# Kernel tuning notes

Measured on AMD Instinct MI355X. Metric: run time of the kernel, lower is better.

## Reference

```python
import jax, jax.numpy as jnp
import numpy as np
from jax import lax

B, PR, PC, IN, E, H = 32, 32, 32, 256, 256, 512  # H2 = 2*H = GRU hidden
H2 = 2 * H
EPS = 1e-5


def setup_inputs() -> dict:
    key = jax.random.key(0)
    ks = jax.random.split(key, 8)
    s = 0.02
    return {
        "x": jax.random.normal(ks[0], (B, PR, PC, IN), jnp.float32),
        "emb_W": jax.random.normal(ks[1], (E, IN), jnp.float32) * s,
        "emb_b": jnp.zeros((E,), jnp.float32),
        "W_ih": jax.random.normal(ks[2], (3 * H2, E), jnp.float32) * s,
        "b_ih": jnp.zeros((3 * H2,), jnp.float32),
        "W_hh": jax.random.normal(ks[3], (3 * H2, H2), jnp.float32) * s,
        "b_hh": jnp.zeros((3 * H2,), jnp.float32),
        "comp_W": jax.random.normal(ks[4], (H, H2), jnp.float32) * s,
        "comp_b": jnp.zeros((H,), jnp.float32),
        "res_W": jax.random.normal(ks[5], (H, E), jnp.float32) * s,
        "res_b": jnp.zeros((H,), jnp.float32),
        "ln_g": jnp.ones((H,), jnp.float32),
        "ln_b": jnp.zeros((H,), jnp.float32),
    }


def reference(x, emb_W, emb_b, W_ih, b_ih, W_hh, b_hh, comp_W, comp_b,
              res_W, res_b, ln_g, ln_b):
    # Embed all cells at once, then precompute input-side GRU gates and residual proj.
    e = jnp.einsum('bijd,ed->bije', x, emb_W) + emb_b          # (B,PR,PC,E)
    gi = jnp.einsum('bije,ge->bijg', e, W_ih) + b_ih            # (B,PR,PC,3*H2)
    res = jnp.einsum('bije,he->bije'.replace('e->','h->')[:0] or 'bije,he->bijh', e, res_W) + res_b  # (B,PR,PC,H)

    def cell(last_col, inputs):
        gi_c, res_c, last_row_c = inputs        # (B,3H2), (B,H), (B,H)
        h_prev = jnp.concatenate([last_row_c, last_col], axis=-1)  # (B,H2)
        gh = h_prev @ W_hh.T + b_hh                                 # (B,3H2)
        ir, iz, inn = jnp.split(gi_c, 3, axis=-1)
        hr, hz, hn = jnp.split(gh, 3, axis=-1)
        r = jax.nn.sigmoid(ir + hr)
        z = jax.nn.sigmoid(iz + hz)
        n = jnp.tanh(inn + r * hn)
        h = (1.0 - z) * n + z * h_prev                              # (B,H2) GRU cell out
        hc = h @ comp_W.T + comp_b + res_c                          # compress + residual
        mu = jnp.mean(hc, axis=-1, keepdims=True)
        var = jnp.var(hc, axis=-1, keepdims=True)
        hn_out = (hc - mu) / jnp.sqrt(var + EPS) * ln_g + ln_b      # LayerNorm
        return hn_out, hn_out

    def row_step(prev_row, row_inputs):
        gi_r, res_r = row_inputs                 # (PC,B,3H2), (PC,B,H)
        last_rows = jnp.swapaxes(prev_row, 0, 1)  # (PC,B,H)
        init_col = jnp.zeros((x.shape[0], H), x.dtype)
        _, row_out = lax.scan(cell, init_col, (gi_r, res_r, last_rows))  # (PC,B,H)
        new_row = jnp.swapaxes(row_out, 0, 1)     # (B,PC,H)
        return new_row, new_row

    gi_s = jnp.transpose(gi, (1, 2, 0, 3))    # (PR,PC,B,3H2)
    res_s = jnp.transpose(res, (1, 2, 0, 3))  # (PR,PC,B,H)
    init_row = jnp.zeros((x.shape[0], x.shape[2], H), x.dtype)
    _, rows = lax.scan(row_step, init_row, (gi_s, res_s))  # (PR,B,PC,H)

    output = jnp.transpose(rows, (1, 0, 2, 3))[None]  # (1,B,PR,PC,H)
    h_final = output[0, :, -1, -1, :]                 # (B,H)
    return output, h_final
```

## Files before the change

kernel.cpp:

```cpp
#include <hip/hip_runtime.h>
#include <hip/hip_fp16.h>

typedef _Float16 h8 __attribute__((ext_vector_type(8)));
typedef _Float16 h4 __attribute__((ext_vector_type(4)));
typedef float f4 __attribute__((ext_vector_type(4)));

#define DEV __device__ __forceinline__

constexpr unsigned kNumBlk = 256u;

DEV float sigm(float x) { return 1.f / (1.f + __expf(-x)); }
DEV float tanhfast(float x) {
    x = fminf(fmaxf(x, -15.f), 15.f);
    float e = __expf(2.f * x);
    return (e - 1.f) / (e + 1.f);
}
DEV h8 h8zero() {
    h8 v;
#pragma unroll
    for (int e = 0; e < 8; ++e) v[e] = (_Float16)0.f;
    return v;
}

DEV void gbar(unsigned* bar, unsigned nblocks) {
    __syncthreads();
    if (threadIdx.x == 0) {
        __threadfence();
        unsigned g = __hip_atomic_load(&bar[1], __ATOMIC_RELAXED, __HIP_MEMORY_SCOPE_AGENT);
        unsigned prev = __hip_atomic_fetch_add(&bar[0], 1u, __ATOMIC_RELAXED, __HIP_MEMORY_SCOPE_AGENT);
        if (prev + 1u == nblocks) {
            __hip_atomic_store(&bar[0], 0u, __ATOMIC_RELAXED, __HIP_MEMORY_SCOPE_AGENT);
            __hip_atomic_store(&bar[1], g + 1u, __ATOMIC_RELEASE, __HIP_MEMORY_SCOPE_AGENT);
        } else {
            unsigned cur;
            do {
                __builtin_amdgcn_s_sleep(2);
                cur = __hip_atomic_load(&bar[1], __ATOMIC_RELAXED, __HIP_MEMORY_SCOPE_AGENT);
            } while (cur == g);
        }
        (void)__hip_atomic_load(&bar[1], __ATOMIC_ACQUIRE, __HIP_MEMORY_SCOPE_AGENT);
    }
    __syncthreads();
}

__global__ void k_zero(unsigned* ptr, int n) {
    int i = blockIdx.x * 256 + threadIdx.x;
    if (i < n) ptr[i] = 0u;
}

__global__ void k_cast_f2h(const float* __restrict__ in, _Float16* __restrict__ out, int n4) {
    int i = blockIdx.x * blockDim.x + threadIdx.x;
    if (i < n4) {
        float4 v = reinterpret_cast<const float4*>(in)[i];
        h4 o;
        o[0] = (_Float16)v.x; o[1] = (_Float16)v.y; o[2] = (_Float16)v.z; o[3] = (_Float16)v.w;
        reinterpret_cast<h4*>(out)[i] = o;
    }
}

__global__ void k_pack_wext(const float* __restrict__ Wih, const float* __restrict__ Whh,
                            _Float16* __restrict__ Wext) {
    int n = blockIdx.x, g = n >> 10, kk = n & 1023;
#pragma unroll
    for (int it = 0; it < 5; ++it) {
        int k = it * 256 + threadIdx.x;
        float v;
        if (k < 1024) v = (g == 3) ? 0.f : Whh[(size_t)(g * 1024 + kk) * 1024 + k];
        else          v = (g == 2) ? 0.f : Wih[(size_t)((g == 3 ? 2048 + kk : g * 1024 + kk)) * 256 + (k - 1024)];
        Wext[(size_t)n * 1280 + k] = (_Float16)v;
    }
}

__global__ void k_pack_cwext(const float* __restrict__ compW, const float* __restrict__ resW,
                             _Float16* __restrict__ cWext) {
    int n = blockIdx.x;
#pragma unroll
    for (int it = 0; it < 5; ++it) {
        int k = it * 256 + threadIdx.x;
        float v = (k < 1024) ? compW[(size_t)n * 1024 + k] : resW[(size_t)n * 256 + (k - 1024)];
        cWext[(size_t)n * 1280 + k] = (_Float16)v;
    }
}

__global__ __launch_bounds__(256, 1) void k_gemm_a32(
    const float* __restrict__ A, const _Float16* __restrict__ W,
    const float* __restrict__ bias, _Float16* __restrict__ C,
    int M, int N, int K, int Ntiles) {
    __shared__ __align__(16) _Float16 sA[128 * 72];
    __shared__ __align__(16) _Float16 sB[128 * 72];
    int tm = blockIdx.x / Ntiles, tn = blockIdx.x % Ntiles;
    int tid = threadIdx.x, lane = tid & 63, w = tid >> 6;
    int wr = w >> 1, wc = w & 1;
    f4 acc[4][4] = {};
    for (int k0 = 0; k0 < K; k0 += 64) {
#pragma unroll
        for (int p = 0; p < 4; ++p) {
            int ch = tid + p * 256;
            int r = ch >> 3, cc = ch & 7;
            const float* ap = A + (size_t)(tm * 128 + r) * K + k0 + cc * 8;
            float4 v0 = *reinterpret_cast<const float4*>(ap);
            float4 v1 = *reinterpret_cast<const float4*>(ap + 4);
            h8 va;
            va[0] = (_Float16)v0.x; va[1] = (_Float16)v0.y; va[2] = (_Float16)v0.z; va[3] = (_Float16)v0.w;
            va[4] = (_Float16)v1.x; va[5] = (_Float16)v1.y; va[6] = (_Float16)v1.z; va[7] = (_Float16)v1.w;
            *reinterpret_cast<h8*>(sA + r * 72 + cc * 8) = va;
            h8 vb = *reinterpret_cast<const h8*>(W + (size_t)(tn * 128 + r) * K + k0 + cc * 8);
            *reinterpret_cast<h8*>(sB + r * 72 + cc * 8) = vb;
        }
        __syncthreads();
#pragma unroll
        for (int kc = 0; kc < 2; ++kc) {
            int ro = lane & 15;
            int ko = kc * 32 + (lane >> 4) * 8;
            h8 af[4], bf[4];
#pragma unroll
            for (int mf = 0; mf < 4; ++mf)
                af[mf] = *reinterpret_cast<const h8*>(sA + (wr * 64 + mf * 16 + ro) * 72 + ko);
#pragma unroll
            for (int nf = 0; nf < 4; ++nf)
                bf[nf] = *reinterpret_cast<const h8*>(sB + (wc * 64 + nf * 16 + ro) * 72 + ko);
#pragma unroll
            for (int mf = 0; mf < 4; ++mf)
#pragma unroll
                for (int nf = 0; nf < 4; ++nf)
                    acc[mf][nf] = __builtin_amdgcn_mfma_f32_16x16x32_f16(af[mf], bf[nf], acc[mf][nf], 0, 0, 0);
        }
        __syncthreads();
    }
#pragma unroll
    for (int nf = 0; nf < 4; ++nf) {
        int col = tn * 128 + wc * 64 + nf * 16 + (lane & 15);
        float bs = bias[col];
#pragma unroll
        for (int mf = 0; mf < 4; ++mf) {
#pragma unroll
            for (int q = 0; q < 4; ++q) {
                int row = tm * 128 + wr * 64 + mf * 16 + (lane >> 4) * 4 + q;
                C[(size_t)row * N + col] = (_Float16)(acc[mf][nf][q] + bs);
            }
        }
    }
}

struct SA { _Float16 A[128 * 72]; _Float16 B[128 * 72]; };
struct SB { _Float16 A[32 * 72]; _Float16 B[64 * 72]; float red[4][32][2]; };
union __align__(16) SM { SA a; SB b; };

__global__ __launch_bounds__(256, 1) void k_recur(
    const _Float16* __restrict__ e_h,
    const _Float16* __restrict__ Wext,
    const _Float16* __restrict__ cWext,
    const float* __restrict__ bih, const float* __restrict__ bhh,
    const float* __restrict__ compb, const float* __restrict__ resb,
    const float* __restrict__ lng, const float* __restrict__ lnb,
    _Float16* __restrict__ hbuf,
    float* __restrict__ out,
    float* __restrict__ hfinal,
    unsigned* bar,
    unsigned* ctr,
    float* gred) {
    __shared__ SM sm;
    const int tid = threadIdx.x, lane = tid & 63, w = tid >> 6;
    const int lane15 = lane & 15, hi = lane >> 4;

    for (int d = 0; d < 63; ++d) {
        int i0 = d > 31 ? d - 31 : 0;
        int i1 = d < 31 ? d : 31;
        int ncells = i1 - i0 + 1;
        int Mt = (ncells + 3) >> 2;

        if ((int)blockIdx.x < Mt * 32) {
            int s = blockIdx.x & 31;
            int mt = blockIdx.x >> 5;
            f4 acc[2][8] = {};
            for (int kt = 0; kt < 20; ++kt) {
                int k0 = kt * 64;
#pragma unroll
                for (int p = 0; p < 4; ++p) {
                    int ch = tid + p * 256;
                    int r = ch >> 3, cc = ch & 7;
                    int m = mt * 128 + r;
                    int c = m >> 5; if (c >= ncells) c = ncells - 1;
                    int b = m & 31;
                    int i = i0 + c, j = d - i;
                    int k = k0 + cc * 8;
                    h8 v;
                    if (k < 1024) {
                        const float* src = nullptr;
                        if (k < 512) {
                            if (i > 0) src = out + (((size_t)(((b * 32 + (i - 1)) * 32) + j)) << 9) + k;
                        } else {
                            if (j > 0) src = out + (((size_t)(((b * 32 + i) * 32) + (j - 1))) << 9) + (k - 512);
                        }
                        if (src) {
                            float4 f0 = *reinterpret_cast<const float4*>(src);
                            float4 f1 = *reinterpret_cast<const float4*>(src + 4);
                            v[0] = (_Float16)f0.x; v[1] = (_Float16)f0.y;
                            v[2] = (_Float16)f0.z; v[3] = (_Float16)f0.w;
                            v[4] = (_Float16)f1.x; v[5] = (_Float16)f1.y;
                            v[6] = (_Float16)f1.z; v[7] = (_Float16)f1.w;
                        } else v = h8zero();
                    } else {
                        v = *reinterpret_cast<const h8*>(e_h + ((size_t)((b * 32 + i) * 32 + j) << 8) + (k - 1024));
                    }
                    *reinterpret_cast<h8*>(sm.a.A + r * 72 + cc * 8) = v;
                }
#pragma unroll
                for (int p = 0; p < 4; ++p) {
                    int ch = tid + p * 256;
                    int rr = ch >> 3, cc = ch & 7;
                    int g = rr >> 5, t = rr & 31;
                    int n = g * 1024 + s * 32 + t;
                    h8 v = *reinterpret_cast<const h8*>(Wext + (size_t)n * 1280 + k0 + cc * 8);
                    *reinterpret_cast<h8*>(sm.a.B + rr * 72 + cc * 8) = v;
                }
                __syncthreads();
#pragma unroll
                for (int kc = 0; kc < 2; ++kc) {
                    int ko = kc * 32 + hi * 8;
                    h8 af[2], bf[8];
#pragma unroll
                    for (int mf = 0; mf < 2; ++mf)
                        af[mf] = *reinterpret_cast<const h8*>(sm.a.A + (w * 32 + mf * 16 + lane15) * 72 + ko);
#pragma unroll
                    for (int nf = 0; nf < 8; ++nf)
                        bf[nf] = *reinterpret_cast<const h8*>(sm.a.B + ((nf >> 1) * 32 + (nf & 1) * 16 + lane15) * 72 + ko);
#pragma unroll
                    for (int mf = 0; mf < 2; ++mf)
#pragma unroll
                        for (int nf = 0; nf < 8; ++nf)
                            acc[mf][nf] = __builtin_amdgcn_mfma_f32_16x16x32_f16(af[mf], bf[nf], acc[mf][nf], 0, 0, 0);
                }
                __syncthreads();
            }
#pragma unroll
            for (int mf = 0; mf < 2; ++mf) {
                int rbase = mt * 128 + w * 32 + mf * 16 + hi * 4;
#pragma unroll
                for (int q = 0; q < 4; ++q) {
                    int m = rbase + q;
                    int c = m >> 5;
                    if (c >= ncells) continue;
                    int b = m & 31;
                    int i = i0 + c, j = d - i;
#pragma unroll
                    for (int u = 0; u < 2; ++u) {
                        int kk = s * 32 + u * 16 + lane15;
                        float r_ = sigm(acc[mf][u][q] + bih[kk] + bhh[kk]);
                        float z_ = sigm(acc[mf][2 + u][q] + bih[1024 + kk] + bhh[1024 + kk]);
                        float hn_ = acc[mf][4 + u][q] + bhh[2048 + kk];
                        float in_ = acc[mf][6 + u][q] + bih[2048 + kk];
                        float hp;
                        if (kk < 512)
                            hp = (i == 0) ? 0.f
                                 : out[(((size_t)(((b * 32 + (i - 1)) * 32) + j)) << 9) + kk];
                        else
                            hp = (j == 0) ? 0.f
                                 : out[(((size_t)(((b * 32 + i) * 32) + (j - 1))) << 9) + kk - 512];
                        float n_ = tanhfast(in_ + r_ * hn_);
                        float h_ = (1.f - z_) * n_ + z_ * hp;
                        hbuf[((size_t)(c * 32 + b) << 10) + kk] = (_Float16)h_;
                    }
                }
            }
        }
        gbar(bar, kNumBlk);

        if ((int)blockIdx.x < ncells * 8) {
            int c = blockIdx.x >> 3, sl = blockIdx.x & 7;
            int i = i0 + c, j = d - i;
            f4 acc[2] = {};
            const _Float16* Ab = hbuf + ((size_t)c << 15);
            for (int kt = 0; kt < 20; ++kt) {
                int k0 = kt * 64;
                {
                    int r = tid >> 3, cc = tid & 7;
                    int k = k0 + cc * 8;
                    h8 v;
                    if (k < 1024) v = *reinterpret_cast<const h8*>(Ab + ((size_t)r << 10) + k);
                    else v = *reinterpret_cast<const h8*>(e_h + ((size_t)((r * 32 + i) * 32 + j) << 8) + (k - 1024));
                    *reinterpret_cast<h8*>(sm.b.A + r * 72 + cc * 8) = v;
                }
#pragma unroll
                for (int p = 0; p < 2; ++p) {
                    int ch = tid + p * 256;
                    int rr = ch >> 3, cc = ch & 7;
                    h8 v = *reinterpret_cast<const h8*>(cWext + (size_t)(sl * 64 + rr) * 1280 + k0 + cc * 8);
                    *reinterpret_cast<h8*>(sm.b.B + rr * 72 + cc * 8) = v;
                }
                __syncthreads();
#pragma unroll
                for (int kc = 0; kc < 2; ++kc) {
                    int ko = kc * 32 + hi * 8;
                    h8 bf = *reinterpret_cast<const h8*>(sm.b.B + (w * 16 + lane15) * 72 + ko);
#pragma unroll
                    for (int mf = 0; mf < 2; ++mf) {
                        h8 af = *reinterpret_cast<const h8*>(sm.b.A + (mf * 16 + lane15) * 72 + ko);
                        acc[mf] = __builtin_amdgcn_mfma_f32_16x16x32_f16(af, bf, acc[mf], 0, 0, 0);
                    }
                }
                __syncthreads();
            }
            int col = sl * 64 + w * 16 + lane15;
            float cb = compb[col] + resb[col];
            float s1[2][4], s2[2][4];
#pragma unroll
            for (int mf = 0; mf < 2; ++mf)
#pragma unroll
                for (int q = 0; q < 4; ++q) {
                    float v = acc[mf][q] + cb;
                    acc[mf][q] = v;
                    s1[mf][q] = v; s2[mf][q] = v * v;
                }
#pragma unroll
            for (int off = 1; off < 16; off <<= 1)
#pragma unroll
                for (int mf = 0; mf < 2; ++mf)
#pragma unroll
                    for (int q = 0; q < 4; ++q) {
                        s1[mf][q] += __shfl_xor(s1[mf][q], off, 64);
                        s2[mf][q] += __shfl_xor(s2[mf][q], off, 64);
                    }
            if (lane15 == 0)
#pragma unroll
                for (int mf = 0; mf < 2; ++mf)
#pragma unroll
                    for (int q = 0; q < 4; ++q) {
                        int b = mf * 16 + hi * 4 + q;
                        sm.b.red[w][b][0] = s1[mf][q];
                        sm.b.red[w][b][1] = s2[mf][q];
                    }
            __syncthreads();
            size_t gbase = (((size_t)d * 32 + c) << 6);
            if (tid < 32) {
                int b = tid;
                float t1 = sm.b.red[0][b][0] + sm.b.red[1][b][0] + sm.b.red[2][b][0] + sm.b.red[3][b][0];
                float t2 = sm.b.red[0][b][1] + sm.b.red[1][b][1] + sm.b.red[2][b][1] + sm.b.red[3][b][1];
                atomicAdd(&gred[gbase + b * 2 + 0], t1);
                atomicAdd(&gred[gbase + b * 2 + 1], t2);
            }
            if (tid == 0) {
                __hip_atomic_fetch_add(&ctr[d * 32 + c], 1u, __ATOMIC_RELEASE, __HIP_MEMORY_SCOPE_AGENT);
                unsigned cur;
                do {
                    __builtin_amdgcn_s_sleep(2);
                    cur = __hip_atomic_load(&ctr[d * 32 + c], __ATOMIC_RELAXED, __HIP_MEMORY_SCOPE_AGENT);
                } while (cur < 8u);
                (void)__hip_atomic_load(&ctr[d * 32 + c], __ATOMIC_ACQUIRE, __HIP_MEMORY_SCOPE_AGENT);
            }
            __syncthreads();
            float lg = lng[col], lb = lnb[col];
#pragma unroll
            for (int mf = 0; mf < 2; ++mf)
#pragma unroll
                for (int q = 0; q < 4; ++q) {
                    int b = mf * 16 + hi * 4 + q;
                    float t1 = gred[gbase + b * 2 + 0];
                    float t2 = gred[gbase + b * 2 + 1];
                    float mu = t1 * (1.f / 512.f);
                    float var = t2 * (1.f / 512.f) - mu * mu;
                    float rstd = rsqrtf(var + 1e-5f);
                    float y = (acc[mf][q] - mu) * rstd * lg + lb;
                    size_t ob = ((size_t)((b * 32 + i) * 32 + j)) << 9;
                    out[ob + col] = y;
                    if (i == 31 && j == 31) hfinal[((size_t)b << 9) + col] = y;
                }
            __syncthreads();
        }
        gbar(bar, kNumBlk);
    }
}

extern "C" void kernel_launch(void* const* d_in, const int* in_sizes, int n_in,
                              void* d_out, int out_size, void* d_ws, size_t ws_size,
                              hipStream_t stream) {
    const float* x = (const float*)d_in[0];
    const float* embW = (const float*)d_in[1];
    const float* embb = (const float*)d_in[2];
    const float* Wih = (const float*)d_in[3];
    const float* bih = (const float*)d_in[4];
    const float* Whh = (const float*)d_in[5];
    const float* bhh = (const float*)d_in[6];
    const float* compW = (const float*)d_in[7];
    const float* compb = (const float*)d_in[8];
    const float* resW = (const float*)d_in[9];
    const float* resb = (const float*)d_in[10];
    const float* lng = (const float*)d_in[11];
    const float* lnb = (const float*)d_in[12];
    float* out = (float*)d_out;
    float* hfinal = out + (size_t)32768 * 512;
    (void)in_sizes; (void)n_in; (void)out_size; (void)ws_size;

    _Float16* p = (_Float16*)d_ws;
    _Float16* e_h = p;    p += 8388608;
    _Float16* embW_h = p; p += 65536;
    _Float16* Wext = p;   p += 5242880;
    _Float16* cWext = p;  p += 655360;
    _Float16* hbuf = p;   p += 1048576;
    unsigned* bar = (unsigned*)p;
    unsigned* ctr = bar + 2;
    float* gred = (float*)(ctr + 63 * 32);
    const int kZeroWords = 2 + 63 * 32 + 63 * 32 * 32 * 2;

    k_zero<<<(kZeroWords + 255) / 256, 256, 0, stream>>>(bar, kZeroWords);
    k_cast_f2h<<<64, 256, 0, stream>>>(embW, embW_h, 16384);
    k_pack_wext<<<4096, 256, 0, stream>>>(Wih, Whh, Wext);
    k_pack_cwext<<<512, 256, 0, stream>>>(compW, resW, cWext);
    k_gemm_a32<<<512, 256, 0, stream>>>(x, embW_h, embb, e_h, 32768, 256, 256, 2);

    k_recur<<<dim3(kNumBlk), dim3(256), 0, stream>>>(
        e_h, Wext, cWext, bih, bhh, compb, resb, lng, lnb,
        hbuf, out, hfinal, bar, ctr, gred);
}
```

Baseline: 6.907 ms.

## Double grid to 512 blocks, add fp16 wavefront buffers, double-buffer tiles, hierarchical barrier

Doubles the persistent grid to 512 blocks with two blocks per CU and halves each block's GEMM tile, so a diagonal's work is spread over more blocks. The previous anti-diagonal's hidden states are stored in a compact fp16 ping-pong buffer, so they no longer have to be re-read from the fp32 output and converted. Both GEMM phases get register-staged double-buffered LDS loads to overlap global loads with MFMA. The grid barrier becomes two-level: eight groups of 64 blocks, then a final count, to reduce atomic contention. The cost is more barrier participants, a smaller tile per block, and the need for two blocks to fit in LDS and registers on each CU.

```diff
diff --git a/kernel.cpp b/kernel.cpp
--- a/kernel.cpp
+++ b/kernel.cpp
@@ -7,7 +7,8 @@
 
 #define DEV __device__ __forceinline__
 
-constexpr unsigned kNumBlk = 256u;
+constexpr unsigned kNumBlk = 512u;
+constexpr int kFrontSz = 32 * 32 * 512;
 
 DEV float sigm(float x) { return 1.f / (1.f + __expf(-x)); }
 DEV float tanhfast(float x) {
@@ -22,23 +23,26 @@
     return v;
 }
 
-DEV void gbar(unsigned* bar, unsigned nblocks) {
+DEV void gbar(unsigned* bar, int grp) {
     __syncthreads();
     if (threadIdx.x == 0) {
         __threadfence();
-        unsigned g = __hip_atomic_load(&bar[1], __ATOMIC_RELAXED, __HIP_MEMORY_SCOPE_AGENT);
-        unsigned prev = __hip_atomic_fetch_add(&bar[0], 1u, __ATOMIC_RELAXED, __HIP_MEMORY_SCOPE_AGENT);
-        if (prev + 1u == nblocks) {
-            __hip_atomic_store(&bar[0], 0u, __ATOMIC_RELAXED, __HIP_MEMORY_SCOPE_AGENT);
-            __hip_atomic_store(&bar[1], g + 1u, __ATOMIC_RELEASE, __HIP_MEMORY_SCOPE_AGENT);
-        } else {
-            unsigned cur;
-            do {
-                __builtin_amdgcn_s_sleep(2);
-                cur = __hip_atomic_load(&bar[1], __ATOMIC_RELAXED, __HIP_MEMORY_SCOPE_AGENT);
-            } while (cur == g);
-        }
-        (void)__hip_atomic_load(&bar[1], __ATOMIC_ACQUIRE, __HIP_MEMORY_SCOPE_AGENT);
+        unsigned g = __hip_atomic_load(&bar[9], __ATOMIC_RELAXED, __HIP_MEMORY_SCOPE_AGENT);
+        unsigned p = __hip_atomic_fetch_add(&bar[grp], 1u, __ATOMIC_ACQ_REL, __HIP_MEMORY_SCOPE_AGENT);
+        if (p == 63u) {
+            __hip_atomic_store(&bar[grp], 0u, __ATOMIC_RELAXED, __HIP_MEMORY_SCOPE_AGENT);
+            unsigned r = __hip_atomic_fetch_add(&bar[8], 1u, __ATOMIC_ACQ_REL, __HIP_MEMORY_SCOPE_AGENT);
+            if (r == 7u) {
+                __hip_atomic_store(&bar[8], 0u, __ATOMIC_RELAXED, __HIP_MEMORY_SCOPE_AGENT);
+                __hip_atomic_store(&bar[9], g + 1u, __ATOMIC_RELEASE, __HIP_MEMORY_SCOPE_AGENT);
+            }
+        }
+        unsigned cur;
+        do {
+            __builtin_amdgcn_s_sleep(2);
+            cur = __hip_atomic_load(&bar[9], __ATOMIC_RELAXED, __HIP_MEMORY_SCOPE_AGENT);
+        } while (cur == g);
+        (void)__hip_atomic_load(&bar[9], __ATOMIC_ACQUIRE, __HIP_MEMORY_SCOPE_AGENT);
     }
     __syncthreads();
 }
@@ -142,11 +146,11 @@
     }
 }
 
-struct SA { _Float16 A[128 * 72]; _Float16 B[128 * 72]; };
-struct SB { _Float16 A[32 * 72]; _Float16 B[64 * 72]; float red[4][32][2]; };
+struct SA { _Float16 A[2][64 * 72]; _Float16 B[2][128 * 72]; };
+struct SB { _Float16 A[2][32 * 72]; _Float16 B[2][32 * 72]; float red[4][32][2]; };
 union __align__(16) SM { SA a; SB b; };
 
-__global__ __launch_bounds__(256, 1) void k_recur(
+__global__ __launch_bounds__(256, 2) void k_recur(
     const _Float16* __restrict__ e_h,
     const _Float16* __restrict__ Wext,
     const _Float16* __restrict__ cWext,
@@ -154,6 +158,7 @@
     const float* __restrict__ compb, const float* __restrict__ resb,
     const float* __restrict__ lng, const float* __restrict__ lnb,
     _Float16* __restrict__ hbuf,
+    _Float16* __restrict__ Hfront,
     float* __restrict__ out,
     float* __restrict__ hfinal,
     unsigned* bar,
@@ -162,180 +167,175 @@
     __shared__ SM sm;
     const int tid = threadIdx.x, lane = tid & 63, w = tid >> 6;
     const int lane15 = lane & 15, hi = lane >> 4;
+    const int bid = blockIdx.x, grp = bid >> 6;
 
     for (int d = 0; d < 63; ++d) {
-        int i0 = d > 31 ? d - 31 : 0;
-        int i1 = d < 31 ? d : 31;
-        int ncells = i1 - i0 + 1;
-        int Mt = (ncells + 3) >> 2;
-
-        if ((int)blockIdx.x < Mt * 32) {
-            int s = blockIdx.x & 31;
-            int mt = blockIdx.x >> 5;
-            f4 acc[2][8] = {};
-            for (int kt = 0; kt < 20; ++kt) {
+        const int i0 = d > 31 ? d - 31 : 0;
+        const int i1 = d < 31 ? d : 31;
+        const int ncells = i1 - i0 + 1;
+        const int i0p = d > 32 ? d - 32 : 0;
+        const _Float16* Hprev = Hfront + ((d & 1) ^ 1) * kFrontSz;
+        _Float16* Hcur = Hfront + (d & 1) * kFrontSz;
+
+        const int Mt2 = (ncells + 1) >> 1;
+        if (bid < Mt2 * 32) {
+            const int s = bid & 31;
+            const int mt = bid >> 5;
+            f4 acc[8] = {};
+            h8 ra[2], rb[4];
+            auto issue = [&](int kt) {
                 int k0 = kt * 64;
 #pragma unroll
-                for (int p = 0; p < 4; ++p) {
+                for (int p = 0; p < 2; ++p) {
                     int ch = tid + p * 256;
                     int r = ch >> 3, cc = ch & 7;
-                    int m = mt * 128 + r;
+                    int m = mt * 64 + r;
                     int c = m >> 5; if (c >= ncells) c = ncells - 1;
                     int b = m & 31;
                     int i = i0 + c, j = d - i;
                     int k = k0 + cc * 8;
-                    h8 v;
-                    if (k < 1024) {
-                        const float* src = nullptr;
-                        if (k < 512) {
-                            if (i > 0) src = out + (((size_t)(((b * 32 + (i - 1)) * 32) + j)) << 9) + k;
-                        } else {
-                            if (j > 0) src = out + (((size_t)(((b * 32 + i) * 32) + (j - 1))) << 9) + (k - 512);
-                        }
-                        if (src) {
-                            float4 f0 = *reinterpret_cast<const float4*>(src);
-                            float4 f1 = *reinterpret_cast<const float4*>(src + 4);
-                            v[0] = (_Float16)f0.x; v[1] = (_Float16)f0.y;
-                            v[2] = (_Float16)f0.z; v[3] = (_Float16)f0.w;
-                            v[4] = (_Float16)f1.x; v[5] = (_Float16)f1.y;
-                            v[6] = (_Float16)f1.z; v[7] = (_Float16)f1.w;
-                        } else v = h8zero();
+                    if (k < 512) {
+                        ra[p] = (i > 0) ? *reinterpret_cast<const h8*>(
+                                    Hprev + (((size_t)((i - 1 - i0p) * 32 + b)) << 9) + k)
+                                        : h8zero();
+                    } else if (k < 1024) {
+                        ra[p] = (j > 0) ? *reinterpret_cast<const h8*>(
+                                    Hprev + (((size_t)((i - i0p) * 32 + b)) << 9) + (k - 512))
+                                        : h8zero();
                     } else {
-                        v = *reinterpret_cast<const h8*>(e_h + ((size_t)((b * 32 + i) * 32 + j) << 8) + (k - 1024));
+                        ra[p] = *reinterpret_cast<const h8*>(
+                            e_h + (((size_t)((b * 32 + i) * 32 + j)) << 8) + (k - 1024));
                     }
-                    *reinterpret_cast<h8*>(sm.a.A + r * 72 + cc * 8) = v;
                 }
 #pragma unroll
                 for (int p = 0; p < 4; ++p) {
                     int ch = tid + p * 256;
                     int rr = ch >> 3, cc = ch & 7;
-                    int g = rr >> 5, t = rr & 31;
-                    int n = g * 1024 + s * 32 + t;
-                    h8 v = *reinterpret_cast<const h8*>(Wext + (size_t)n * 1280 + k0 + cc * 8);
-                    *reinterpret_cast<h8*>(sm.a.B + rr * 72 + cc * 8) = v;
-                }
-                __syncthreads();
+                    int n = (rr >> 5) * 1024 + s * 32 + (rr & 31);
+                    rb[p] = *reinterpret_cast<const h8*>(Wext + (size_t)n * 1280 + k0 + cc * 8);
+                }
+            };
+            auto commit = [&](int buf) {
+#pragma unroll
+                for (int p = 0; p < 2; ++p) {
+                    int ch = tid + p * 256;
+                    int r = ch >> 3, cc = ch & 7;
+                    *reinterpret_cast<h8*>(sm.a.A[buf] + r * 72 + cc * 8) = ra[p];
+                }
+#pragma unroll
+                for (int p = 0; p < 4; ++p) {
+                    int ch = tid + p * 256;
+                    int rr = ch >> 3, cc = ch & 7;
+                    *reinterpret_cast<h8*>(sm.a.B[buf] + rr * 72 + cc * 8) = rb[p];
+                }
+            };
+            issue(0); commit(0); __syncthreads();
+            for (int kt = 0; kt < 20; ++kt) {
+                int cur = kt & 1;
+                if (kt < 19) issue(kt + 1);
 #pragma unroll
                 for (int kc = 0; kc < 2; ++kc) {
                     int ko = kc * 32 + hi * 8;
-                    h8 af[2], bf[8];
-#pragma unroll
-                    for (int mf = 0; mf < 2; ++mf)
-                        af[mf] = *reinterpret_cast<const h8*>(sm.a.A + (w * 32 + mf * 16 + lane15) * 72 + ko);
-#pragma unroll
-                    for (int nf = 0; nf < 8; ++nf)
-                        bf[nf] = *reinterpret_cast<const h8*>(sm.a.B + ((nf >> 1) * 32 + (nf & 1) * 16 + lane15) * 72 + ko);
-#pragma unroll
-                    for (int mf = 0; mf < 2; ++mf)
-#pragma unroll
-                        for (int nf = 0; nf < 8; ++nf)
-                            acc[mf][nf] = __builtin_amdgcn_mfma_f32_16x16x32_f16(af[mf], bf[nf], acc[mf][nf], 0, 0, 0);
-                }
-                __syncthreads();
-            }
-#pragma unroll
-            for (int mf = 0; mf < 2; ++mf) {
-                int rbase = mt * 128 + w * 32 + mf * 16 + hi * 4;
+                    h8 af = *reinterpret_cast<const h8*>(sm.a.A[cur] + (w * 16 + lane15) * 72 + ko);
+#pragma unroll
+                    for (int nf = 0; nf < 8; ++nf) {
+                        h8 bf = *reinterpret_cast<const h8*>(
+                            sm.a.B[cur] + ((nf >> 1) * 32 + (nf & 1) * 16 + lane15) * 72 + ko);
+                        acc[nf] = __builtin_amdgcn_mfma_f32_16x16x32_f16(af, bf, acc[nf], 0, 0, 0);
+                    }
+                }
+                if (kt < 19) { commit(cur ^ 1); __syncthreads(); }
+            }
+            int rbase = mt * 64 + w * 16 + hi * 4;
+            int c = (rbase >> 5);
+            if (c < ncells) {
+                int i = i0 + c, j = d - i;
 #pragma unroll
                 for (int q = 0; q < 4; ++q) {
-                    int m = rbase + q;
-                    int c = m >> 5;
-                    if (c >= ncells) continue;
-                    int b = m & 31;
-                    int i = i0 + c, j = d - i;
+                    int b = (rbase + q) & 31;
 #pragma unroll
                     for (int u = 0; u < 2; ++u) {
                         int kk = s * 32 + u * 16 + lane15;
-                        float r_ = sigm(acc[mf][u][q] + bih[kk] + bhh[kk]);
-                        float z_ = sigm(acc[mf][2 + u][q] + bih[1024 + kk] + bhh[1024 + kk]);
-                        float hn_ = acc[mf][4 + u][q] + bhh[2048 + kk];
-                        float in_ = acc[mf][6 + u][q] + bih[2048 + kk];
+                        float r_ = sigm(acc[u][q] + bih[kk] + bhh[kk]);
+                        float z_ = sigm(acc[2 + u][q] + bih[1024 + kk] + bhh[1024 + kk]);
+                        float hn_ = acc[4 + u][q] + bhh[2048 + kk];
+                        float in_ = acc[6 + u][q] + bih[2048 + kk];
                         float hp;
                         if (kk < 512)
-                            hp = (i == 0) ? 0.f
-                                 : out[(((size_t)(((b * 32 + (i - 1)) * 32) + j)) << 9) + kk];
+                            hp = (i > 0) ? (float)Hprev[(((size_t)((i - 1 - i0p) * 32 + b)) << 9) + kk] : 0.f;
                         else
-                            hp = (j == 0) ? 0.f
-                                 : out[(((size_t)(((b * 32 + i) * 32) + (j - 1))) << 9) + kk - 512];
+                            hp = (j > 0) ? (float)Hprev[(((size_t)((i - i0p) * 32 + b)) << 9) + kk - 512] : 0.f;
                         float n_ = tanhfast(in_ + r_ * hn_);
                         float h_ = (1.f - z_) * n_ + z_ * hp;
-                        hbuf[((size_t)(c * 32 + b) << 10) + kk] = (_Float16)h_;
+                        hbuf[(((size_t)(c * 32 + b)) << 10) + kk] = (_Float16)h_;
                     }
                 }
             }
         }
-        gbar(bar, kNumBlk);
-
-        if ((int)blockIdx.x < ncells * 8) {
-            int c = blockIdx.x >> 3, sl = blockIdx.x & 7;
-            int i = i0 + c, j = d - i;
-            f4 acc[2] = {};
-            const _Float16* Ab = hbuf + ((size_t)c << 15);
+        gbar(bar, grp);
+
+        if (bid < ncells * 16) {
+            const int c = bid >> 4, sl = bid & 15;
+            const int i = i0 + c, j = d - i;
+            const int mf = w >> 1, nf = w & 1;
+            f4 acc = {};
+            h8 rA, rB;
+            auto issueB = [&](int kt) {
+                int k0 = kt * 64;
+                int r = tid >> 3, cc = tid & 7;
+                int k = k0 + cc * 8;
+                rA = (k < 1024)
+                    ? *reinterpret_cast<const h8*>(hbuf + (((size_t)(c * 32 + r)) << 10) + k)
+                    : *reinterpret_cast<const h8*>(e_h + (((size_t)((r * 32 + i) * 32 + j)) << 8) + (k - 1024));
+                rB = *reinterpret_cast<const h8*>(cWext + (size_t)(sl * 32 + r) * 1280 + k0 + cc * 8);
+            };
+            auto commitB = [&](int buf) {
+                int r = tid >> 3, cc = tid & 7;
+                *reinterpret_cast<h8*>(sm.b.A[buf] + r * 72 + cc * 8) = rA;
+                *reinterpret_cast<h8*>(sm.b.B[buf] + r * 72 + cc * 8) = rB;
+            };
+            issueB(0); commitB(0); __syncthreads();
             for (int kt = 0; kt < 20; ++kt) {
-                int k0 = kt * 64;
-                {
-                    int r = tid >> 3, cc = tid & 7;
-                    int k = k0 + cc * 8;
-                    h8 v;
-                    if (k < 1024) v = *reinterpret_cast<const h8*>(Ab + ((size_t)r << 10) + k);
-                    else v = *reinterpret_cast<const h8*>(e_h + ((size_t)((r * 32 + i) * 32 + j) << 8) + (k - 1024));
-                    *reinterpret_cast<h8*>(sm.b.A + r * 72 + cc * 8) = v;
-                }
-#pragma unroll
-                for (int p = 0; p < 2; ++p) {
-                    int ch = tid + p * 256;
-                    int rr = ch >> 3, cc = ch & 7;
-                    h8 v = *reinterpret_cast<const h8*>(cWext + (size_t)(sl * 64 + rr) * 1280 + k0 + cc * 8);
-                    *reinterpret_cast<h8*>(sm.b.B + rr * 72 + cc * 8) = v;
-                }
-                __syncthreads();
+                int cur = kt & 1;
+                if (kt < 19) issueB(kt + 1);
 #pragma unroll
                 for (int kc = 0; kc < 2; ++kc) {
                     int ko = kc * 32 + hi * 8;
-                    h8 bf = *reinterpret_cast<const h8*>(sm.b.B + (w * 16 + lane15) * 72 + ko);
-#pragma unroll
-                    for (int mf = 0; mf < 2; ++mf) {
-                        h8 af = *reinterpret_cast<const h8*>(sm.b.A + (mf * 16 + lane15) * 72 + ko);
-                        acc[mf] = __builtin_amdgcn_mfma_f32_16x16x32_f16(af, bf, acc[mf], 0, 0, 0);
-                    }
-                }
-                __syncthreads();
-            }
-            int col = sl * 64 + w * 16 + lane15;
+                    h8 af = *reinterpret_cast<const h8*>(sm.b.A[cur] + (mf * 16 + lane15) * 72 + ko);
+                    h8 bf = *reinterpret_cast<const h8*>(sm.b.B[cur] + (nf * 16 + lane15) * 72 + ko);
+                    acc = __builtin_amdgcn_mfma_f32_16x16x32_f16(af, bf, acc, 0, 0, 0);
+                }
+                if (kt < 19) { commitB(cur ^ 1); __syncthreads(); }
+            }
+            int col = sl * 32 + nf * 16 + lane15;
             float cb = compb[col] + resb[col];
-            float s1[2][4], s2[2][4];
-#pragma unroll
-            for (int mf = 0; mf < 2; ++mf)
+            float s1v[4], s2v[4];
+#pragma unroll
+            for (int q = 0; q < 4; ++q) {
+                float v = acc[q] + cb;
+                acc[q] = v;
+                s1v[q] = v; s2v[q] = v * v;
+            }
+#pragma unroll
+            for (int off = 1; off < 16; off <<= 1)
 #pragma unroll
                 for (int q = 0; q < 4; ++q) {
-                    float v = acc[mf][q] + cb;
-                    acc[mf][q] = v;
-                    s1[mf][q] = v; s2[mf][q] = v * v;
-                }
-#pragma unroll
-            for (int off = 1; off < 16; off <<= 1)
-#pragma unroll
-                for (int mf = 0; mf < 2; ++mf)
-#pragma unroll
-                    for (int q = 0; q < 4; ++q) {
-                        s1[mf][q] += __shfl_xor(s1[mf][q], off, 64);
-                        s2[mf][q] += __shfl_xor(s2[mf][q], off, 64);
-                    }
+                    s1v[q] += __shfl_xor(s1v[q], off, 64);
+                    s2v[q] += __shfl_xor(s2v[q], off, 64);
+                }
             if (lane15 == 0)
 #pragma unroll
-                for (int mf = 0; mf < 2; ++mf)
-#pragma unroll
-                    for (int q = 0; q < 4; ++q) {
-                        int b = mf * 16 + hi * 4 + q;
-                        sm.b.red[w][b][0] = s1[mf][q];
-                        sm.b.red[w][b][1] = s2[mf][q];
-                    }
+                for (int q = 0; q < 4; ++q) {
+                    int b = mf * 16 + hi * 4 + q;
+                    sm.b.red[w][b][0] = s1v[q];
+                    sm.b.red[w][b][1] = s2v[q];
+                }
             __syncthreads();
             size_t gbase = (((size_t)d * 32 + c) << 6);
             if (tid < 32) {
-                int b = tid;
-                float t1 = sm.b.red[0][b][0] + sm.b.red[1][b][0] + sm.b.red[2][b][0] + sm.b.red[3][b][0];
-                float t2 = sm.b.red[0][b][1] + sm.b.red[1][b][1] + sm.b.red[2][b][1] + sm.b.red[3][b][1];
+                int b = tid, wb = (b >> 4) * 2;
+                float t1 = sm.b.red[wb][b][0] + sm.b.red[wb + 1][b][0];
+                float t2 = sm.b.red[wb][b][1] + sm.b.red[wb + 1][b][1];
                 atomicAdd(&gred[gbase + b * 2 + 0], t1);
                 atomicAdd(&gred[gbase + b * 2 + 1], t2);
             }
@@ -345,29 +345,26 @@
                 do {
                     __builtin_amdgcn_s_sleep(2);
                     cur = __hip_atomic_load(&ctr[d * 32 + c], __ATOMIC_RELAXED, __HIP_MEMORY_SCOPE_AGENT);
-                } while (cur < 8u);
+                } while (cur < 16u);
                 (void)__hip_atomic_load(&ctr[d * 32 + c], __ATOMIC_ACQUIRE, __HIP_MEMORY_SCOPE_AGENT);
             }
             __syncthreads();
             float lg = lng[col], lb = lnb[col];
 #pragma unroll
-            for (int mf = 0; mf < 2; ++mf)
-#pragma unroll
-                for (int q = 0; q < 4; ++q) {
-                    int b = mf * 16 + hi * 4 + q;
-                    float t1 = gred[gbase + b * 2 + 0];
-                    float t2 = gred[gbase + b * 2 + 1];
-                    float mu = t1 * (1.f / 512.f);
-                    float var = t2 * (1.f / 512.f) - mu * mu;
-                    float rstd = rsqrtf(var + 1e-5f);
-                    float y = (acc[mf][q] - mu) * rstd * lg + lb;
-                    size_t ob = ((size_t)((b * 32 + i) * 32 + j)) << 9;
-                    out[ob + col] = y;
-                    if (i == 31 && j == 31) hfinal[((size_t)b << 9) + col] = y;
-                }
-            __syncthreads();
-        }
-        gbar(bar, kNumBlk);
+            for (int q = 0; q < 4; ++q) {
+                int b = mf * 16 + hi * 4 + q;
+                float t1 = gred[gbase + b * 2 + 0];
+                float t2 = gred[gbase + b * 2 + 1];
+                float mu = t1 * (1.f / 512.f);
+                float var = t2 * (1.f / 512.f) - mu * mu;
+                float rstd = rsqrtf(var + 1e-5f);
+                float y = (acc[q] - mu) * rstd * lg + lb;
+                out[(((size_t)((b * 32 + i) * 32 + j)) << 9) + col] = y;
+                Hcur[(((size_t)(c * 32 + b)) << 9) + col] = (_Float16)y;
+                if (i == 31 && j == 31) hfinal[((size_t)b << 9) + col] = y;
+            }
+        }
+        gbar(bar, grp);
     }
 }
 
@@ -397,10 +394,11 @@
     _Float16* Wext = p;   p += 5242880;
     _Float16* cWext = p;  p += 655360;
     _Float16* hbuf = p;   p += 1048576;
+    _Float16* Hfront = p; p += 2 * kFrontSz;
     unsigned* bar = (unsigned*)p;
-    unsigned* ctr = bar + 2;
+    unsigned* ctr = bar + 10;
     float* gred = (float*)(ctr + 63 * 32);
-    const int kZeroWords = 2 + 63 * 32 + 63 * 32 * 32 * 2;
+    const int kZeroWords = 10 + 63 * 32 + 63 * 32 * 32 * 2;
 
     k_zero<<<(kZeroWords + 255) / 256, 256, 0, stream>>>(bar, kZeroWords);
     k_cast_f2h<<<64, 256, 0, stream>>>(embW, embW_h, 16384);
@@ -410,5 +408,5 @@
 
     k_recur<<<dim3(kNumBlk), dim3(256), 0, stream>>>(
         e_h, Wext, cWext, bih, bhh, compb, resb, lng, lnb,
-        hbuf, out, hfinal, bar, ctr, gred);
-}
+        hbuf, Hfront, out, hfinal, bar, ctr, gred);
+}
```

After: 10.41 ms. 1.51x slower.
